# Performance work log

Measured on AMD Instinct MI355X. Metric: run time of the kernel, lower is better.

## Reference

```python
import jax, jax.numpy as jnp
import numpy as np

BINS = 256
MAXV = float(2 ** 14 - 1)
LAP_K = jnp.array([[0.0, 1.0, 0.0], [1.0, -4.0, 1.0], [0.0, 1.0, 0.0]], jnp.float32).reshape(1, 1, 3, 3)


def _soft_hist_entropy(flat):
    # flat: (B, N) in arbitrary range; per-image min-max normalize to [0,1]
    fmin = jnp.min(flat, axis=1, keepdims=True)
    fmax = jnp.max(flat, axis=1, keepdims=True)
    rng = fmax - fmin
    rng = jnp.where(rng == 0, jnp.ones_like(rng), rng)
    x = jnp.clip((flat - fmin) / rng, 0.0, 1.0)
    # Triangular soft-histogram weights clamp(1-|x-c_k|/bw, 0) are nonzero for at
    # most the 2 bins adjacent to x, so scatter-add instead of a (B,N,BINS) tensor.
    p = x * BINS - 0.5            # position in bin-center coordinates
    i0 = jnp.floor(p)
    w1 = p - i0                   # weight on bin i0+1
    w0 = 1.0 - w1                 # weight on bin i0
    i0i = i0.astype(jnp.int32)
    i1i = i0i + 1
    v0 = (i0i >= 0) & (i0i < BINS)
    v1 = (i1i >= 0) & (i1i < BINS)

    def hist_one(idx0, idx1, a0, a1, m0, m1):
        h = jnp.zeros((BINS,), flat.dtype)
        h = h.at[jnp.clip(idx0, 0, BINS - 1)].add(jnp.where(m0, a0, 0.0))
        h = h.at[jnp.clip(idx1, 0, BINS - 1)].add(jnp.where(m1, a1, 0.0))
        return h

    hist = jax.vmap(hist_one)(i0i, i1i, w0, w1, v0, v1)  # (B, BINS)
    hist = hist / (jnp.sum(hist, axis=1, keepdims=True) + 1e-10)
    ent = -jnp.sum(hist * jnp.log2(hist + 1e-10), axis=1)
    return ent / jnp.float32(np.log2(BINS))


def _extract_features(image):
    # normalize 14-bit input to [0,1] iff values exceed 1 (matches torch branch)
    image = jnp.where(jnp.max(image) > 1.0, image / MAXV, image)
    B = image.shape[0]
    flat = image.reshape(B, -1)
    variance = jnp.var(flat, axis=1, ddof=1)   # torch.var is unbiased
    mn = jnp.min(flat, axis=1)
    mx = jnp.max(flat, axis=1)
    ent = _soft_hist_entropy(flat)
    lap = jax.lax.conv_general_dilated(
        image, LAP_K, window_strides=(1, 1), padding=[(1, 1), (1, 1)],
        dimension_numbers=('NCHW', 'OIHW', 'NCHW'))
    lap_var = jnp.var(lap.reshape(B, -1), axis=1, ddof=1)
    return jnp.stack([variance, mn, mx, ent, lap_var], axis=1)  # (B, 5)


def setup_inputs() -> dict:
    key = jax.random.key(0)
    ks = jax.random.split(key, 4)
    image = jax.random.uniform(ks[0], (16, 1, 1024, 1280), jnp.float32) * MAXV
    # Kaiming normal fan_in (relu): std = sqrt(2 / fan_in); biases zero
    W1 = jax.random.normal(ks[1], (64, 5), jnp.float32) * np.float32(np.sqrt(2.0 / 5))
    W2 = jax.random.normal(ks[2], (64, 64), jnp.float32) * np.float32(np.sqrt(2.0 / 64))
    W3 = jax.random.normal(ks[3], (3, 64), jnp.float32) * np.float32(np.sqrt(2.0 / 64))
    return {
        'image': image,
        'W1': W1, 'b1': jnp.zeros((64,), jnp.float32),
        'W2': W2, 'b2': jnp.zeros((64,), jnp.float32),
        'W3': W3, 'b3': jnp.zeros((3,), jnp.float32),
    }


def reference(image, W1, b1, W2, b2, W3, b3):
    feats = _extract_features(image)                       # (B, 5)
    h = jax.nn.relu(feats @ W1.T + b1)
    h = jax.nn.relu(h @ W2.T + b2)
    logits = h @ W3.T + b3                                  # (B, 3)
    probs = jax.nn.softmax(logits, axis=1)
    class_ids = jnp.argmax(probs, axis=1)
    return class_ids, probs, feats
```

## Files before the change

kernel.cpp:

```cpp
#include <hip/hip_runtime.h>
#include <cfloat>
#include <math.h>

#define IMG_B 16
#define IMG_H 1024
#define IMG_W 1280
#define NPIX (IMG_H * IMG_W)
#define BINS 256
#define ROWS_PER_BLOCK 16
#define BLOCKS_PER_IMG_P1 (IMG_H / ROWS_PER_BLOCK)
#define T1 (IMG_W / 4)
#define BPI2 64
#define FIXP 65536.0f

__device__ __forceinline__ unsigned encf(float f) {
    unsigned u = __float_as_uint(f);
    return (u >> 31) ? ~u : (u | 0x80000000u);
}
__device__ __forceinline__ float decf(unsigned u) {
    unsigned b = (u & 0x80000000u) ? (u & 0x7fffffffu) : ~u;
    return __uint_as_float(b);
}


__global__ __launch_bounds__(256) void k_init(unsigned* mm, unsigned long long* hist64) {
    int t = blockIdx.x * 256 + threadIdx.x;
    hist64[t] = 0ull;
    if (t < IMG_B) { mm[2 * t] = 0xFFFFFFFFu; mm[2 * t + 1] = 0u; }
}

__global__ __launch_bounds__(T1) void k_pass1(const float* __restrict__ img,
                                              double* __restrict__ partials,
                                              unsigned* __restrict__ mm) {
    int blk = blockIdx.x;
    int b   = blk >> 6;
    int r0  = (blk & 63) * ROWS_PER_BLOCK;
    const float* base = img + (size_t)b * NPIX;
    int c = threadIdx.x;

    float fmn = FLT_MAX, fmx = -FLT_MAX;
    double s = 0.0, s2 = 0.0, ls = 0.0, ls2 = 0.0;

    for (int i = 0; i < ROWS_PER_BLOCK; ++i) {
        int r = r0 + i;
        const float* rowf = base + (size_t)r * IMG_W;
        float4 m = ((const float4*)rowf)[c];
        float4 up = make_float4(0.f, 0.f, 0.f, 0.f);
        float4 dn = make_float4(0.f, 0.f, 0.f, 0.f);
        if (r > 0)          up = ((const float4*)(rowf - IMG_W))[c];
        if (r < IMG_H - 1)  dn = ((const float4*)(rowf + IMG_W))[c];
        float lft = (c > 0)      ? rowf[4 * c - 1] : 0.f;
        float rgt = (c < T1 - 1) ? rowf[4 * c + 4] : 0.f;

        fmn = fminf(fmn, fminf(fminf(m.x, m.y), fminf(m.z, m.w)));
        fmx = fmaxf(fmx, fmaxf(fmaxf(m.x, m.y), fmaxf(m.z, m.w)));
        s  += (double)m.x + (double)m.y + (double)m.z + (double)m.w;
        s2 += (double)m.x * m.x + (double)m.y * m.y + (double)m.z * m.z + (double)m.w * m.w;

        float l0 = up.x + dn.x + lft + m.y - 4.f * m.x;
        float l1 = up.y + dn.y + m.x + m.z - 4.f * m.y;
        float l2 = up.z + dn.z + m.y + m.w - 4.f * m.z;
        float l3 = up.w + dn.w + m.z + rgt - 4.f * m.w;
        ls  += (double)l0 + (double)l1 + (double)l2 + (double)l3;
        ls2 += (double)l0 * l0 + (double)l1 * l1 + (double)l2 * l2 + (double)l3 * l3;
    }

    for (int o = 32; o; o >>= 1) {
        s   += __shfl_down(s,   (unsigned)o, 64);
        s2  += __shfl_down(s2,  (unsigned)o, 64);
        ls  += __shfl_down(ls,  (unsigned)o, 64);
        ls2 += __shfl_down(ls2, (unsigned)o, 64);
        fmn = fminf(fmn, __shfl_down(fmn, (unsigned)o, 64));
        fmx = fmaxf(fmx, __shfl_down(fmx, (unsigned)o, 64));
    }
    __shared__ double rd[4][5];
    __shared__ float  rf[2][5];
    int lane = threadIdx.x & 63, wv = threadIdx.x >> 6;
    if (lane == 0) {
        rd[0][wv] = s; rd[1][wv] = s2; rd[2][wv] = ls; rd[3][wv] = ls2;
        rf[0][wv] = fmn; rf[1][wv] = fmx;
    }
    __syncthreads();
    if (threadIdx.x == 0) {
        double S = 0, S2 = 0, LS = 0, LS2 = 0;
        float mn = FLT_MAX, mx = -FLT_MAX;
        for (int i = 0; i < 5; ++i) {
            S += rd[0][i]; S2 += rd[1][i]; LS += rd[2][i]; LS2 += rd[3][i];
            mn = fminf(mn, rf[0][i]); mx = fmaxf(mx, rf[1][i]);
        }
        double* p = partials + (size_t)blk * 4;
        p[0] = S; p[1] = S2; p[2] = LS; p[3] = LS2;
        atomicMin(&mm[b * 2 + 0], encf(mn));
        atomicMax(&mm[b * 2 + 1], encf(mx));
    }
}

__global__ __launch_bounds__(256) void k_pass2(const float* __restrict__ img,
                                               const unsigned* __restrict__ mm,
                                               unsigned long long* __restrict__ hist64) {
    __shared__ unsigned lh[BINS];
    int b     = blockIdx.x / BPI2;
    int blkin = blockIdx.x % BPI2;
    lh[threadIdx.x] = 0u;
    __syncthreads();

    float fmn = decf(mm[b * 2 + 0]);
    float fmx = decf(mm[b * 2 + 1]);
    float rng = fmx - fmn;
    if (rng == 0.f) rng = 1.f;
    float inv = 1.f / rng;

    const float4* p = (const float4*)(img + (size_t)b * NPIX);
    int nf4 = NPIX / 4;
    for (int i = blkin * 256 + threadIdx.x; i < nf4; i += BPI2 * 256) {
        float4 v = p[i];
        #pragma unroll
        for (int j = 0; j < 4; ++j) {
            float vv = (j == 0) ? v.x : (j == 1) ? v.y : (j == 2) ? v.z : v.w;
            float x  = fminf(fmaxf((vv - fmn) * inv, 0.f), 1.f);
            float pp = x * 256.f - 0.5f;
            float fi = floorf(pp);
            int   i0 = (int)fi;
            float w1 = pp - fi;
            unsigned w1q = (unsigned)(w1 * FIXP + 0.5f);
            unsigned w0q = 65536u - w1q;
            if (i0 >= 0)       atomicAdd(&lh[i0], w0q);
            if (i0 < BINS - 1) atomicAdd(&lh[i0 + 1], w1q);
        }
    }
    __syncthreads();
    unsigned hv = lh[threadIdx.x];
    if (hv != 0u)
        atomicAdd(&hist64[b * BINS + threadIdx.x], (unsigned long long)hv);
}

__global__ __launch_bounds__(256) void k_pass3(const unsigned long long* __restrict__ hist64,
                                               const double* __restrict__ partials,
                                               const unsigned* __restrict__ mm,
                                               float* __restrict__ featsw,
                                               float* __restrict__ out) {
    int b = blockIdx.x, t = threadIdx.x;
    double h = (double)hist64[b * BINS + t] * (1.0 / 65536.0);

    __shared__ double red[4];
    __shared__ float red2[4];
    __shared__ double mom[4];
    double tot = h;
    for (int o = 32; o; o >>= 1) tot += __shfl_down(tot, (unsigned)o, 64);
    if ((t & 63) == 0) red[t >> 6] = tot;

    if (t < 64) {
        const double* p = partials + ((size_t)b * 64 + t) * 4;
        double q0 = p[0], q1 = p[1], q2 = p[2], q3 = p[3];
        for (int o = 32; o; o >>= 1) {
            q0 += __shfl_down(q0, (unsigned)o, 64);
            q1 += __shfl_down(q1, (unsigned)o, 64);
            q2 += __shfl_down(q2, (unsigned)o, 64);
            q3 += __shfl_down(q3, (unsigned)o, 64);
        }
        if (t == 0) { mom[0] = q0; mom[1] = q1; mom[2] = q2; mom[3] = q3; }
    }
    __syncthreads();
    double tot_all = red[0] + red[1] + red[2] + red[3];

    float hn = (float)(h / (tot_all + 1e-10));
    float ce = hn * log2f(hn + 1e-10f);
    for (int o = 32; o; o >>= 1) ce += __shfl_down(ce, (unsigned)o, 64);
    if ((t & 63) == 0) red2[t >> 6] = ce;
    __syncthreads();

    if (t == 0) {
        float ent = -(red2[0] + red2[1] + red2[2] + red2[3]) / 8.f;
        float gmax = -FLT_MAX;
        for (int i = 0; i < IMG_B; ++i) gmax = fmaxf(gmax, decf(mm[i * 2 + 1]));
        float sc = (gmax > 1.f) ? (1.f / 16383.f) : 1.f;
        double N = (double)NPIX;
        double S = mom[0], S2 = mom[1], LS = mom[2], LS2 = mom[3];
        double sc2 = (double)sc * (double)sc;
        float var  = (float)((S2  - S  * S  / N) / (N - 1.0) * sc2);
        float lvar = (float)((LS2 - LS * LS / N) / (N - 1.0) * sc2);
        float mn = decf(mm[b * 2 + 0]) * sc;
        float mx = decf(mm[b * 2 + 1]) * sc;
        float* fo = out + 16 + 48 + b * 5;
        fo[0] = var; fo[1] = mn; fo[2] = mx; fo[3] = ent; fo[4] = lvar;
        float* fw = featsw + b * 5;
        fw[0] = var; fw[1] = mn; fw[2] = mx; fw[3] = ent; fw[4] = lvar;
    }
}

__global__ __launch_bounds__(64) void k_pass4(const float* __restrict__ feats,
                                              const float* __restrict__ W1, const float* __restrict__ b1,
                                              const float* __restrict__ W2, const float* __restrict__ b2,
                                              const float* __restrict__ W3, const float* __restrict__ b3,
                                              float* __restrict__ out) {
    int t = threadIdx.x;
    int b = blockIdx.x;
    __shared__ float f[5], h1[64], h2[64], lg[3];
    if (t < 5) f[t] = feats[b * 5 + t];
    __syncthreads();
    float a = b1[t];
    #pragma unroll
    for (int k = 0; k < 5; ++k) a += W1[t * 5 + k] * f[k];
    h1[t] = fmaxf(a, 0.f);
    __syncthreads();
    float a2 = b2[t];
    #pragma unroll
    for (int k = 0; k < 64; ++k) a2 += W2[t * 64 + k] * h1[k];
    h2[t] = fmaxf(a2, 0.f);
    __syncthreads();
    if (t < 3) {
        float a3 = b3[t];
        #pragma unroll
        for (int k = 0; k < 64; ++k) a3 += W3[t * 64 + k] * h2[k];
        lg[t] = a3;
    }
    __syncthreads();
    if (t == 0) {
        float m = fmaxf(lg[0], fmaxf(lg[1], lg[2]));
        float e0 = expf(lg[0] - m), e1 = expf(lg[1] - m), e2 = expf(lg[2] - m);
        float inv = 1.f / (e0 + e1 + e2);
        float p0 = e0 * inv, p1 = e1 * inv, p2 = e2 * inv;
        out[16 + b * 3 + 0] = p0;
        out[16 + b * 3 + 1] = p1;
        out[16 + b * 3 + 2] = p2;
        int cid = 0; float bm = p0;
        if (p1 > bm) { bm = p1; cid = 1; }
        if (p2 > bm) { bm = p2; cid = 2; }
        out[b] = (float)cid;
    }
}

extern "C" void kernel_launch(void* const* d_in, const int* in_sizes, int n_in,
                              void* d_out, int out_size, void* d_ws, size_t ws_size,
                              hipStream_t stream) {
    const float* img = (const float*)d_in[0];
    const float* W1  = (const float*)d_in[1];
    const float* b1  = (const float*)d_in[2];
    const float* W2  = (const float*)d_in[3];
    const float* b2  = (const float*)d_in[4];
    const float* W3  = (const float*)d_in[5];
    const float* b3  = (const float*)d_in[6];
    float* out = (float*)d_out;

    char* ws = (char*)d_ws;
    double*             partials = (double*)ws;
    unsigned*           mm       = (unsigned*)(ws + 32768);
    unsigned long long* hist64   = (unsigned long long*)(ws + 32896);
    float*              featsw   = (float*)(ws + 65664);

    k_init <<<16, 256, 0, stream>>>(mm, hist64);
    k_pass1<<<IMG_B * BLOCKS_PER_IMG_P1, T1, 0, stream>>>(img, partials, mm);
    k_pass2<<<IMG_B * BPI2, 256, 0, stream>>>(img, mm, hist64);
    k_pass3<<<IMG_B, 256, 0, stream>>>(hist64, partials, mm, featsw, out);
    k_pass4<<<IMG_B, 64, 0, stream>>>(featsw, W1, b1, W2, b2, W3, b3, out);
}
```

Baseline: 175.1 us.

## Fuse all passes into one cooperative kernel with grid syncs

Replaces the five-kernel chain with a single cooperative kernel of 1024 blocks that uses grid.sync between the moments/min-max stage, the histogram stage and the per-image finalize plus MLP head. Per-block partial histograms and min/max are written to workspace and reduced by the finalize blocks, which removes the global 64-bit atomics and the init kernel. The moment pass now accumulates in float per thread with register rows and wave shuffles for the left/right neighbours instead of double accumulation. This trades launch overhead and atomics for grid-wide barriers, reduced-precision partial sums, and a dependence on the cooperative launch succeeding; the old path remains as a fallback.

```diff
diff --git a/kernel.cpp b/kernel.cpp
--- a/kernel.cpp
+++ b/kernel.cpp
@@ -1,16 +1,17 @@
 #include <hip/hip_runtime.h>
+#include <hip/hip_cooperative_groups.h>
 #include <cfloat>
 #include <math.h>
+
+namespace cg = cooperative_groups;
 
 #define IMG_B 16
 #define IMG_H 1024
 #define IMG_W 1280
 #define NPIX (IMG_H * IMG_W)
 #define BINS 256
-#define ROWS_PER_BLOCK 16
-#define BLOCKS_PER_IMG_P1 (IMG_H / ROWS_PER_BLOCK)
-#define T1 (IMG_W / 4)
-#define BPI2 64
+#define NBLK 1024
+#define NTHR 256
 #define FIXP 65536.0f
 
 __device__ __forceinline__ unsigned encf(float f) {
@@ -22,6 +23,258 @@
     return __uint_as_float(b);
 }
 
+
+__global__ __launch_bounds__(NTHR, 4) void k_fused(
+    const float* __restrict__ img,
+    const float* __restrict__ W1, const float* __restrict__ b1,
+    const float* __restrict__ W2, const float* __restrict__ b2,
+    const float* __restrict__ W3, const float* __restrict__ b3,
+    float* __restrict__ out,
+    double* __restrict__ mom, uint2* __restrict__ mmp,
+    unsigned* __restrict__ bhist)
+{
+    cg::grid_group grid = cg::this_grid();
+    const int blk  = blockIdx.x;
+    const int tid  = threadIdx.x;
+    const int b    = blk >> 6;
+    const int sl   = blk & 63;
+    const int lane = tid & 63;
+    const int wv   = tid >> 6;
+
+    __shared__ float    swred[6][4];
+    __shared__ unsigned lh[BINS];
+    __shared__ float    sh_mm[2];
+    __shared__ double   dred[4];
+    __shared__ float    fred[4];
+    __shared__ double   smom[4];
+    __shared__ unsigned smm2[2];
+    __shared__ unsigned sgm[4];
+    __shared__ float    f5[5], h1[64], h2[64], lg[3];
+
+    const float* base = img + (size_t)b * NPIX;
+
+    {
+        float fs = 0.f, fs2 = 0.f, fls = 0.f, fls2 = 0.f;
+        float fmn = FLT_MAX, fmx = -FLT_MAX;
+
+        const int r0 = sl * 16 + wv * 4;
+        const float4* rp = (const float4*)(base + (size_t)r0 * IMG_W);
+        float4 up[5], m[5], dn[5];
+        #pragma unroll
+        for (int k = 0; k < 5; ++k) {
+            int c = k * 64 + lane;
+            up[k] = (r0 > 0) ? rp[c - 320] : make_float4(0.f, 0.f, 0.f, 0.f);
+            m[k]  = rp[c];
+        }
+        #pragma unroll
+        for (int i = 0; i < 4; ++i) {
+            int r = r0 + i;
+            const float4* nr = (const float4*)(base + (size_t)(r + 1) * IMG_W);
+            #pragma unroll
+            for (int k = 0; k < 5; ++k)
+                dn[k] = (r < IMG_H - 1) ? nr[k * 64 + lane]
+                                        : make_float4(0.f, 0.f, 0.f, 0.f);
+            #pragma unroll
+            for (int k = 0; k < 5; ++k) {
+                float4 mm = m[k], u = up[k], d = dn[k];
+                float lin  = __shfl_up(mm.w, 1u, 64);
+                float lwr  = m[k ? k - 1 : 0].w;
+                lwr = __shfl(lwr, 63, 64);
+                float lft  = (lane == 0) ? ((k > 0) ? lwr : 0.f) : lin;
+                float rin  = __shfl_down(mm.x, 1u, 64);
+                float rwr  = m[k < 4 ? k + 1 : 4].x;
+                rwr = __shfl(rwr, 0, 64);
+                float rgt  = (lane == 63) ? ((k < 4) ? rwr : 0.f) : rin;
+
+                float l0 = u.x + d.x + lft  + mm.y - 4.f * mm.x;
+                float l1 = u.y + d.y + mm.x + mm.z - 4.f * mm.y;
+                float l2 = u.z + d.z + mm.y + mm.w - 4.f * mm.z;
+                float l3 = u.w + d.w + mm.z + rgt  - 4.f * mm.w;
+
+                fs   += (mm.x + mm.y) + (mm.z + mm.w);
+                fs2  += mm.x * mm.x + mm.y * mm.y + mm.z * mm.z + mm.w * mm.w;
+                fls  += (l0 + l1) + (l2 + l3);
+                fls2 += l0 * l0 + l1 * l1 + l2 * l2 + l3 * l3;
+                fmn = fminf(fmn, fminf(fminf(mm.x, mm.y), fminf(mm.z, mm.w)));
+                fmx = fmaxf(fmx, fmaxf(fmaxf(mm.x, mm.y), fmaxf(mm.z, mm.w)));
+            }
+            #pragma unroll
+            for (int k = 0; k < 5; ++k) { up[k] = m[k]; m[k] = dn[k]; }
+        }
+
+        for (int o = 32; o; o >>= 1) {
+            fs   += __shfl_down(fs,   (unsigned)o, 64);
+            fs2  += __shfl_down(fs2,  (unsigned)o, 64);
+            fls  += __shfl_down(fls,  (unsigned)o, 64);
+            fls2 += __shfl_down(fls2, (unsigned)o, 64);
+            fmn = fminf(fmn, __shfl_down(fmn, (unsigned)o, 64));
+            fmx = fmaxf(fmx, __shfl_down(fmx, (unsigned)o, 64));
+        }
+        if (lane == 0) {
+            swred[0][wv] = fs;  swred[1][wv] = fs2;
+            swred[2][wv] = fls; swred[3][wv] = fls2;
+            swred[4][wv] = fmn; swred[5][wv] = fmx;
+        }
+        __syncthreads();
+        if (tid == 0) {
+            double S = 0, S2 = 0, LS = 0, LS2 = 0;
+            float mn = FLT_MAX, mx = -FLT_MAX;
+            for (int i = 0; i < 4; ++i) {
+                S  += (double)swred[0][i]; S2  += (double)swred[1][i];
+                LS += (double)swred[2][i]; LS2 += (double)swred[3][i];
+                mn = fminf(mn, swred[4][i]); mx = fmaxf(mx, swred[5][i]);
+            }
+            mom[blk * 4 + 0] = S;  mom[blk * 4 + 1] = S2;
+            mom[blk * 4 + 2] = LS; mom[blk * 4 + 3] = LS2;
+            mmp[blk] = make_uint2(encf(mn), encf(mx));
+        }
+    }
+    __threadfence();
+    grid.sync();
+
+    {
+        if (tid < 64) {
+            uint2 e = mmp[b * 64 + tid];
+            unsigned emn = e.x, emx = e.y;
+            for (int o = 32; o; o >>= 1) {
+                emn = min(emn, (unsigned)__shfl_down(emn, (unsigned)o, 64));
+                emx = max(emx, (unsigned)__shfl_down(emx, (unsigned)o, 64));
+            }
+            if (tid == 0) { sh_mm[0] = decf(emn); sh_mm[1] = decf(emx); }
+        }
+        lh[tid] = 0u;
+        __syncthreads();
+
+        float fmn = sh_mm[0], fmx = sh_mm[1];
+        float rng = fmx - fmn;
+        if (rng == 0.f) rng = 1.f;
+        float inv = 1.f / rng;
+
+        const float4* p = (const float4*)base + (size_t)sl * 5120;
+        #pragma unroll 4
+        for (int i = tid; i < 5120; i += NTHR) {
+            float4 v = p[i];
+            #pragma unroll
+            for (int j = 0; j < 4; ++j) {
+                float vv = (j == 0) ? v.x : (j == 1) ? v.y : (j == 2) ? v.z : v.w;
+                float x  = fminf(fmaxf((vv - fmn) * inv, 0.f), 1.f);
+                float pp = x * 256.f - 0.5f;
+                float fi = floorf(pp);
+                int   i0 = (int)fi;
+                float w1 = pp - fi;
+                unsigned w1q = (unsigned)(w1 * FIXP + 0.5f);
+                unsigned w0q = 65536u - w1q;
+                if (i0 >= 0)        atomicAdd(&lh[i0], w0q);
+                if (i0 < BINS - 1)  atomicAdd(&lh[i0 + 1], w1q);
+            }
+        }
+        __syncthreads();
+        bhist[blk * BINS + tid] = lh[tid];
+    }
+    __threadfence();
+    grid.sync();
+
+    if (blk >= IMG_B) return;
+    const int ib = blk;
+
+    double h = 0.0;
+    for (int s = 0; s < 64; ++s)
+        h += (double)bhist[(ib * 64 + s) * BINS + tid];
+
+    double tot = h;
+    for (int o = 32; o; o >>= 1) tot += __shfl_down(tot, (unsigned)o, 64);
+    if (lane == 0) dred[wv] = tot;
+    __syncthreads();
+    tot = dred[0] + dred[1] + dred[2] + dred[3];
+
+    double hv = h * (1.0 / 65536.0);
+    double tv = tot * (1.0 / 65536.0);
+    float hn = (float)(hv / (tv + 1e-10));
+    float ce = hn * log2f(hn + 1e-10f);
+    for (int o = 32; o; o >>= 1) ce += __shfl_down(ce, (unsigned)o, 64);
+    if (lane == 0) fred[wv] = ce;
+
+    if (tid < 64) {
+        double q0 = mom[(ib * 64 + tid) * 4 + 0];
+        double q1 = mom[(ib * 64 + tid) * 4 + 1];
+        double q2 = mom[(ib * 64 + tid) * 4 + 2];
+        double q3 = mom[(ib * 64 + tid) * 4 + 3];
+        uint2 e = mmp[ib * 64 + tid];
+        unsigned emn = e.x, emx = e.y;
+        for (int o = 32; o; o >>= 1) {
+            q0 += __shfl_down(q0, (unsigned)o, 64);
+            q1 += __shfl_down(q1, (unsigned)o, 64);
+            q2 += __shfl_down(q2, (unsigned)o, 64);
+            q3 += __shfl_down(q3, (unsigned)o, 64);
+            emn = min(emn, (unsigned)__shfl_down(emn, (unsigned)o, 64));
+            emx = max(emx, (unsigned)__shfl_down(emx, (unsigned)o, 64));
+        }
+        if (tid == 0) {
+            smom[0] = q0; smom[1] = q1; smom[2] = q2; smom[3] = q3;
+            smm2[0] = emn; smm2[1] = emx;
+        }
+    }
+    {
+        unsigned g = max(max(mmp[tid].y, mmp[256 + tid].y),
+                         max(mmp[512 + tid].y, mmp[768 + tid].y));
+        for (int o = 32; o; o >>= 1)
+            g = max(g, (unsigned)__shfl_down(g, (unsigned)o, 64));
+        if (lane == 0) sgm[wv] = g;
+    }
+    __syncthreads();
+
+    if (tid == 0) {
+        float ent = -(fred[0] + fred[1] + fred[2] + fred[3]) / 8.f;
+        float gmax = decf(max(max(sgm[0], sgm[1]), max(sgm[2], sgm[3])));
+        float sc = (gmax > 1.f) ? (1.f / 16383.f) : 1.f;
+        double N = (double)NPIX;
+        double S = smom[0], S2 = smom[1], LS = smom[2], LS2 = smom[3];
+        double sc2 = (double)sc * (double)sc;
+        float var  = (float)((S2  - S  * S  / N) / (N - 1.0) * sc2);
+        float lvar = (float)((LS2 - LS * LS / N) / (N - 1.0) * sc2);
+        float mn = decf(smm2[0]) * sc;
+        float mx = decf(smm2[1]) * sc;
+        float* fo = out + 64 + ib * 5;
+        fo[0] = var; fo[1] = mn; fo[2] = mx; fo[3] = ent; fo[4] = lvar;
+        f5[0] = var; f5[1] = mn; f5[2] = mx; f5[3] = ent; f5[4] = lvar;
+    }
+    __syncthreads();
+
+    if (tid < 64) {
+        float a = b1[tid];
+        #pragma unroll
+        for (int k = 0; k < 5; ++k) a += W1[tid * 5 + k] * f5[k];
+        h1[tid] = fmaxf(a, 0.f);
+    }
+    __syncthreads();
+    if (tid < 64) {
+        float a2 = b2[tid];
+        #pragma unroll
+        for (int k = 0; k < 64; ++k) a2 += W2[tid * 64 + k] * h1[k];
+        h2[tid] = fmaxf(a2, 0.f);
+    }
+    __syncthreads();
+    if (tid < 3) {
+        float a3 = b3[tid];
+        #pragma unroll
+        for (int k = 0; k < 64; ++k) a3 += W3[tid * 64 + k] * h2[k];
+        lg[tid] = a3;
+    }
+    __syncthreads();
+    if (tid == 0) {
+        float m = fmaxf(lg[0], fmaxf(lg[1], lg[2]));
+        float e0 = expf(lg[0] - m), e1 = expf(lg[1] - m), e2 = expf(lg[2] - m);
+        float inv = 1.f / (e0 + e1 + e2);
+        float p0 = e0 * inv, p1 = e1 * inv, p2 = e2 * inv;
+        out[16 + ib * 3 + 0] = p0;
+        out[16 + ib * 3 + 1] = p1;
+        out[16 + ib * 3 + 2] = p2;
+        int cid = 0; float bm = p0;
+        if (p1 > bm) { bm = p1; cid = 1; }
+        if (p2 > bm) { bm = p2; cid = 2; }
+        out[ib] = (float)cid;
+    }
+}
 
 __global__ __launch_bounds__(256) void k_init(unsigned* mm, unsigned long long* hist64) {
     int t = blockIdx.x * 256 + threadIdx.x;
@@ -29,19 +282,19 @@
     if (t < IMG_B) { mm[2 * t] = 0xFFFFFFFFu; mm[2 * t + 1] = 0u; }
 }
 
-__global__ __launch_bounds__(T1) void k_pass1(const float* __restrict__ img,
-                                              double* __restrict__ partials,
-                                              unsigned* __restrict__ mm) {
+__global__ __launch_bounds__(320) void k_pass1(const float* __restrict__ img,
+                                               double* __restrict__ partials,
+                                               unsigned* __restrict__ mm) {
     int blk = blockIdx.x;
     int b   = blk >> 6;
-    int r0  = (blk & 63) * ROWS_PER_BLOCK;
+    int r0  = (blk & 63) * 16;
     const float* base = img + (size_t)b * NPIX;
     int c = threadIdx.x;
 
     float fmn = FLT_MAX, fmx = -FLT_MAX;
     double s = 0.0, s2 = 0.0, ls = 0.0, ls2 = 0.0;
 
-    for (int i = 0; i < ROWS_PER_BLOCK; ++i) {
+    for (int i = 0; i < 16; ++i) {
         int r = r0 + i;
         const float* rowf = base + (size_t)r * IMG_W;
         float4 m = ((const float4*)rowf)[c];
@@ -49,8 +302,8 @@
         float4 dn = make_float4(0.f, 0.f, 0.f, 0.f);
         if (r > 0)          up = ((const float4*)(rowf - IMG_W))[c];
         if (r < IMG_H - 1)  dn = ((const float4*)(rowf + IMG_W))[c];
-        float lft = (c > 0)      ? rowf[4 * c - 1] : 0.f;
-        float rgt = (c < T1 - 1) ? rowf[4 * c + 4] : 0.f;
+        float lft = (c > 0)   ? rowf[4 * c - 1] : 0.f;
+        float rgt = (c < 319) ? rowf[4 * c + 4] : 0.f;
 
         fmn = fminf(fmn, fminf(fminf(m.x, m.y), fminf(m.z, m.w)));
         fmx = fmaxf(fmx, fmaxf(fmaxf(m.x, m.y), fmaxf(m.z, m.w)));
@@ -64,7 +317,6 @@
         ls  += (double)l0 + (double)l1 + (double)l2 + (double)l3;
         ls2 += (double)l0 * l0 + (double)l1 * l1 + (double)l2 * l2 + (double)l3 * l3;
     }
-
     for (int o = 32; o; o >>= 1) {
         s   += __shfl_down(s,   (unsigned)o, 64);
         s2  += __shfl_down(s2,  (unsigned)o, 64);
@@ -99,20 +351,17 @@
                                                const unsigned* __restrict__ mm,
                                                unsigned long long* __restrict__ hist64) {
     __shared__ unsigned lh[BINS];
-    int b     = blockIdx.x / BPI2;
-    int blkin = blockIdx.x % BPI2;
+    int b     = blockIdx.x / 64;
+    int blkin = blockIdx.x % 64;
     lh[threadIdx.x] = 0u;
     __syncthreads();
-
     float fmn = decf(mm[b * 2 + 0]);
     float fmx = decf(mm[b * 2 + 1]);
     float rng = fmx - fmn;
     if (rng == 0.f) rng = 1.f;
     float inv = 1.f / rng;
-
     const float4* p = (const float4*)(img + (size_t)b * NPIX);
-    int nf4 = NPIX / 4;
-    for (int i = blkin * 256 + threadIdx.x; i < nf4; i += BPI2 * 256) {
+    for (int i = blkin * 256 + threadIdx.x; i < NPIX / 4; i += 64 * 256) {
         float4 v = p[i];
         #pragma unroll
         for (int j = 0; j < 4; ++j) {
@@ -141,14 +390,12 @@
                                                float* __restrict__ out) {
     int b = blockIdx.x, t = threadIdx.x;
     double h = (double)hist64[b * BINS + t] * (1.0 / 65536.0);
-
     __shared__ double red[4];
     __shared__ float red2[4];
-    __shared__ double mom[4];
+    __shared__ double momx[4];
     double tot = h;
     for (int o = 32; o; o >>= 1) tot += __shfl_down(tot, (unsigned)o, 64);
     if ((t & 63) == 0) red[t >> 6] = tot;
-
     if (t < 64) {
         const double* p = partials + ((size_t)b * 64 + t) * 4;
         double q0 = p[0], q1 = p[1], q2 = p[2], q3 = p[3];
@@ -158,30 +405,28 @@
             q2 += __shfl_down(q2, (unsigned)o, 64);
             q3 += __shfl_down(q3, (unsigned)o, 64);
         }
-        if (t == 0) { mom[0] = q0; mom[1] = q1; mom[2] = q2; mom[3] = q3; }
+        if (t == 0) { momx[0] = q0; momx[1] = q1; momx[2] = q2; momx[3] = q3; }
     }
     __syncthreads();
     double tot_all = red[0] + red[1] + red[2] + red[3];
-
     float hn = (float)(h / (tot_all + 1e-10));
     float ce = hn * log2f(hn + 1e-10f);
     for (int o = 32; o; o >>= 1) ce += __shfl_down(ce, (unsigned)o, 64);
     if ((t & 63) == 0) red2[t >> 6] = ce;
     __syncthreads();
-
     if (t == 0) {
         float ent = -(red2[0] + red2[1] + red2[2] + red2[3]) / 8.f;
         float gmax = -FLT_MAX;
         for (int i = 0; i < IMG_B; ++i) gmax = fmaxf(gmax, decf(mm[i * 2 + 1]));
         float sc = (gmax > 1.f) ? (1.f / 16383.f) : 1.f;
         double N = (double)NPIX;
-        double S = mom[0], S2 = mom[1], LS = mom[2], LS2 = mom[3];
+        double S = momx[0], S2 = momx[1], LS = momx[2], LS2 = momx[3];
         double sc2 = (double)sc * (double)sc;
         float var  = (float)((S2  - S  * S  / N) / (N - 1.0) * sc2);
         float lvar = (float)((LS2 - LS * LS / N) / (N - 1.0) * sc2);
         float mn = decf(mm[b * 2 + 0]) * sc;
         float mx = decf(mm[b * 2 + 1]) * sc;
-        float* fo = out + 16 + 48 + b * 5;
+        float* fo = out + 64 + b * 5;
         fo[0] = var; fo[1] = mn; fo[2] = mx; fo[3] = ent; fo[4] = lvar;
         float* fw = featsw + b * 5;
         fw[0] = var; fw[1] = mn; fw[2] = mx; fw[3] = ent; fw[4] = lvar;
@@ -243,14 +488,25 @@
     float* out = (float*)d_out;
 
     char* ws = (char*)d_ws;
-    double*             partials = (double*)ws;
-    unsigned*           mm       = (unsigned*)(ws + 32768);
-    unsigned long long* hist64   = (unsigned long long*)(ws + 32896);
-    float*              featsw   = (float*)(ws + 65664);
-
-    k_init <<<16, 256, 0, stream>>>(mm, hist64);
-    k_pass1<<<IMG_B * BLOCKS_PER_IMG_P1, T1, 0, stream>>>(img, partials, mm);
-    k_pass2<<<IMG_B * BPI2, 256, 0, stream>>>(img, mm, hist64);
-    k_pass3<<<IMG_B, 256, 0, stream>>>(hist64, partials, mm, featsw, out);
-    k_pass4<<<IMG_B, 64, 0, stream>>>(featsw, W1, b1, W2, b2, W3, b3, out);
-}
+    double*   mom   = (double*)ws;
+    uint2*    mmp   = (uint2*)(ws + 32768);
+    unsigned* bhist = (unsigned*)(ws + 40960);
+
+    void* kargs[] = {(void*)&img, (void*)&W1, (void*)&b1, (void*)&W2, (void*)&b2,
+                     (void*)&W3, (void*)&b3, (void*)&out, (void*)&mom, (void*)&mmp,
+                     (void*)&bhist};
+    hipError_t err = hipLaunchCooperativeKernel((const void*)k_fused,
+                                                dim3(NBLK), dim3(NTHR),
+                                                kargs, 0, stream);
+    if (err != hipSuccess) {
+        double*             partials = (double*)ws;
+        unsigned*           mm       = (unsigned*)(ws + 32768);
+        unsigned long long* hist64   = (unsigned long long*)(ws + 32896);
+        float*              featsw   = (float*)(ws + 65664);
+        k_init <<<16, 256, 0, stream>>>(mm, hist64);
+        k_pass1<<<IMG_B * 64, 320, 0, stream>>>(img, partials, mm);
+        k_pass2<<<IMG_B * 64, 256, 0, stream>>>(img, mm, hist64);
+        k_pass3<<<IMG_B, 256, 0, stream>>>(hist64, partials, mm, featsw, out);
+        k_pass4<<<IMG_B, 64, 0, stream>>>(featsw, W1, b1, W2, b2, W3, b3, out);
+    }
+}
```

Measured after the change: 596.9 us. +241.0%, slower.

## Restructure pipeline into minmax, fused moments+histogram, and fused final kernel

Applied to the files above, without the earlier changes.

Splits the work into a light min/max pass and a main pass that computes moments, Laplacian moments and the soft histogram from one read of each pixel, removing the separate histogram pass over the image. Global atomics and the init kernel are replaced by per-block partial outputs that the final kernel reduces, and the feature and MLP kernels are merged into one. Moment accumulation moves from double to float per thread, which cuts double-precision cost but may lose accuracy. The image is still read twice in total, but the second read is shared between the statistics and histogram work.

```diff
diff --git a/kernel.cpp b/kernel.cpp
--- a/kernel.cpp
+++ b/kernel.cpp
@@ -7,10 +7,9 @@
 #define IMG_W 1280
 #define NPIX (IMG_H * IMG_W)
 #define BINS 256
-#define ROWS_PER_BLOCK 16
-#define BLOCKS_PER_IMG_P1 (IMG_H / ROWS_PER_BLOCK)
-#define T1 (IMG_W / 4)
-#define BPI2 64
+#define SLICES 64
+#define NBLK (IMG_B * SLICES)
+#define F4_PER_SLICE (16 * IMG_W / 4)
 #define FIXP 65536.0f
 
 __device__ __forceinline__ unsigned encf(float f) {
@@ -23,100 +22,98 @@
 }
 
 
-__global__ __launch_bounds__(256) void k_init(unsigned* mm, unsigned long long* hist64) {
-    int t = blockIdx.x * 256 + threadIdx.x;
-    hist64[t] = 0ull;
-    if (t < IMG_B) { mm[2 * t] = 0xFFFFFFFFu; mm[2 * t + 1] = 0u; }
-}
-
-__global__ __launch_bounds__(T1) void k_pass1(const float* __restrict__ img,
-                                              double* __restrict__ partials,
-                                              unsigned* __restrict__ mm) {
-    int blk = blockIdx.x;
-    int b   = blk >> 6;
-    int r0  = (blk & 63) * ROWS_PER_BLOCK;
+__global__ __launch_bounds__(256) void k_minmax(const float* __restrict__ img,
+                                                uint2* __restrict__ mmp) {
+    const int blk = blockIdx.x;
+    const int tid = threadIdx.x;
+    const float4* p = (const float4*)img + (size_t)blk * F4_PER_SLICE;
+
+    float fmn = FLT_MAX, fmx = -FLT_MAX;
+    #pragma unroll 4
+    for (int i = tid; i < F4_PER_SLICE; i += 256) {
+        float4 v = p[i];
+        fmn = fminf(fmn, fminf(fminf(v.x, v.y), fminf(v.z, v.w)));
+        fmx = fmaxf(fmx, fmaxf(fmaxf(v.x, v.y), fmaxf(v.z, v.w)));
+    }
+    for (int o = 32; o; o >>= 1) {
+        fmn = fminf(fmn, __shfl_down(fmn, (unsigned)o, 64));
+        fmx = fmaxf(fmx, __shfl_down(fmx, (unsigned)o, 64));
+    }
+    __shared__ float rmn[4], rmx[4];
+    int lane = tid & 63, wv = tid >> 6;
+    if (lane == 0) { rmn[wv] = fmn; rmx[wv] = fmx; }
+    __syncthreads();
+    if (tid == 0) {
+        float mn = fminf(fminf(rmn[0], rmn[1]), fminf(rmn[2], rmn[3]));
+        float mx = fmaxf(fmaxf(rmx[0], rmx[1]), fmaxf(rmx[2], rmx[3]));
+        mmp[blk] = make_uint2(encf(mn), encf(mx));
+    }
+}
+
+__global__ __launch_bounds__(256) void k_main(const float* __restrict__ img,
+                                              const uint2* __restrict__ mmp,
+                                              double* __restrict__ mom,
+                                              unsigned* __restrict__ bhist) {
+    const int blk = blockIdx.x;
+    const int tid = threadIdx.x;
+    const int b   = blk >> 6;
+    const int sl  = blk & 63;
+    const int lane = tid & 63, wv = tid >> 6;
+
+    __shared__ unsigned lh[BINS];
+    __shared__ float sh_mm[2];
+    __shared__ float swred[4][4];
+
+    if (tid < 64) {
+        uint2 e = mmp[b * 64 + tid];
+        unsigned emn = e.x, emx = e.y;
+        for (int o = 32; o; o >>= 1) {
+            emn = min(emn, (unsigned)__shfl_down(emn, (unsigned)o, 64));
+            emx = max(emx, (unsigned)__shfl_down(emx, (unsigned)o, 64));
+        }
+        if (tid == 0) { sh_mm[0] = decf(emn); sh_mm[1] = decf(emx); }
+    }
+    lh[tid] = 0u;
+    __syncthreads();
+
+    const float fmn = sh_mm[0], fmx = sh_mm[1];
+    float rng = fmx - fmn;
+    if (rng == 0.f) rng = 1.f;
+    const float inv = 1.f / rng;
+
     const float* base = img + (size_t)b * NPIX;
-    int c = threadIdx.x;
-
-    float fmn = FLT_MAX, fmx = -FLT_MAX;
-    double s = 0.0, s2 = 0.0, ls = 0.0, ls2 = 0.0;
-
-    for (int i = 0; i < ROWS_PER_BLOCK; ++i) {
-        int r = r0 + i;
+    const int r0 = sl * 16;
+
+    float fs = 0.f, fs2 = 0.f, fls = 0.f, fls2 = 0.f;
+
+    #pragma unroll 2
+    for (int k = 0; k < 20; ++k) {
+        int i   = tid + k * 256;
+        int ri  = i / 320;
+        int c   = i - ri * 320;
+        int r   = r0 + ri;
         const float* rowf = base + (size_t)r * IMG_W;
         float4 m = ((const float4*)rowf)[c];
         float4 up = make_float4(0.f, 0.f, 0.f, 0.f);
         float4 dn = make_float4(0.f, 0.f, 0.f, 0.f);
         if (r > 0)          up = ((const float4*)(rowf - IMG_W))[c];
         if (r < IMG_H - 1)  dn = ((const float4*)(rowf + IMG_W))[c];
-        float lft = (c > 0)      ? rowf[4 * c - 1] : 0.f;
-        float rgt = (c < T1 - 1) ? rowf[4 * c + 4] : 0.f;
-
-        fmn = fminf(fmn, fminf(fminf(m.x, m.y), fminf(m.z, m.w)));
-        fmx = fmaxf(fmx, fmaxf(fmaxf(m.x, m.y), fmaxf(m.z, m.w)));
-        s  += (double)m.x + (double)m.y + (double)m.z + (double)m.w;
-        s2 += (double)m.x * m.x + (double)m.y * m.y + (double)m.z * m.z + (double)m.w * m.w;
+        float lft = (c > 0)   ? rowf[4 * c - 1] : 0.f;
+        float rgt = (c < 319) ? rowf[4 * c + 4] : 0.f;
+
+        fs  += (m.x + m.y) + (m.z + m.w);
+        fs2 += (m.x * m.x + m.y * m.y) + (m.z * m.z + m.w * m.w);
 
         float l0 = up.x + dn.x + lft + m.y - 4.f * m.x;
         float l1 = up.y + dn.y + m.x + m.z - 4.f * m.y;
         float l2 = up.z + dn.z + m.y + m.w - 4.f * m.z;
         float l3 = up.w + dn.w + m.z + rgt - 4.f * m.w;
-        ls  += (double)l0 + (double)l1 + (double)l2 + (double)l3;
-        ls2 += (double)l0 * l0 + (double)l1 * l1 + (double)l2 * l2 + (double)l3 * l3;
-    }
-
-    for (int o = 32; o; o >>= 1) {
-        s   += __shfl_down(s,   (unsigned)o, 64);
-        s2  += __shfl_down(s2,  (unsigned)o, 64);
-        ls  += __shfl_down(ls,  (unsigned)o, 64);
-        ls2 += __shfl_down(ls2, (unsigned)o, 64);
-        fmn = fminf(fmn, __shfl_down(fmn, (unsigned)o, 64));
-        fmx = fmaxf(fmx, __shfl_down(fmx, (unsigned)o, 64));
-    }
-    __shared__ double rd[4][5];
-    __shared__ float  rf[2][5];
-    int lane = threadIdx.x & 63, wv = threadIdx.x >> 6;
-    if (lane == 0) {
-        rd[0][wv] = s; rd[1][wv] = s2; rd[2][wv] = ls; rd[3][wv] = ls2;
-        rf[0][wv] = fmn; rf[1][wv] = fmx;
-    }
-    __syncthreads();
-    if (threadIdx.x == 0) {
-        double S = 0, S2 = 0, LS = 0, LS2 = 0;
-        float mn = FLT_MAX, mx = -FLT_MAX;
-        for (int i = 0; i < 5; ++i) {
-            S += rd[0][i]; S2 += rd[1][i]; LS += rd[2][i]; LS2 += rd[3][i];
-            mn = fminf(mn, rf[0][i]); mx = fmaxf(mx, rf[1][i]);
-        }
-        double* p = partials + (size_t)blk * 4;
-        p[0] = S; p[1] = S2; p[2] = LS; p[3] = LS2;
-        atomicMin(&mm[b * 2 + 0], encf(mn));
-        atomicMax(&mm[b * 2 + 1], encf(mx));
-    }
-}
-
-__global__ __launch_bounds__(256) void k_pass2(const float* __restrict__ img,
-                                               const unsigned* __restrict__ mm,
-                                               unsigned long long* __restrict__ hist64) {
-    __shared__ unsigned lh[BINS];
-    int b     = blockIdx.x / BPI2;
-    int blkin = blockIdx.x % BPI2;
-    lh[threadIdx.x] = 0u;
-    __syncthreads();
-
-    float fmn = decf(mm[b * 2 + 0]);
-    float fmx = decf(mm[b * 2 + 1]);
-    float rng = fmx - fmn;
-    if (rng == 0.f) rng = 1.f;
-    float inv = 1.f / rng;
-
-    const float4* p = (const float4*)(img + (size_t)b * NPIX);
-    int nf4 = NPIX / 4;
-    for (int i = blkin * 256 + threadIdx.x; i < nf4; i += BPI2 * 256) {
-        float4 v = p[i];
+        fls  += (l0 + l1) + (l2 + l3);
+        fls2 += (l0 * l0 + l1 * l1) + (l2 * l2 + l3 * l3);
+
         #pragma unroll
         for (int j = 0; j < 4; ++j) {
-            float vv = (j == 0) ? v.x : (j == 1) ? v.y : (j == 2) ? v.z : v.w;
+            float vv = (j == 0) ? m.x : (j == 1) ? m.y : (j == 2) ? m.z : m.w;
             float x  = fminf(fmaxf((vv - fmn) * inv, 0.f), 1.f);
             float pp = x * 256.f - 0.5f;
             float fi = floorf(pp);
@@ -124,109 +121,148 @@
             float w1 = pp - fi;
             unsigned w1q = (unsigned)(w1 * FIXP + 0.5f);
             unsigned w0q = 65536u - w1q;
-            if (i0 >= 0)       atomicAdd(&lh[i0], w0q);
-            if (i0 < BINS - 1) atomicAdd(&lh[i0 + 1], w1q);
-        }
-    }
-    __syncthreads();
-    unsigned hv = lh[threadIdx.x];
-    if (hv != 0u)
-        atomicAdd(&hist64[b * BINS + threadIdx.x], (unsigned long long)hv);
-}
-
-__global__ __launch_bounds__(256) void k_pass3(const unsigned long long* __restrict__ hist64,
-                                               const double* __restrict__ partials,
-                                               const unsigned* __restrict__ mm,
-                                               float* __restrict__ featsw,
-                                               float* __restrict__ out) {
-    int b = blockIdx.x, t = threadIdx.x;
-    double h = (double)hist64[b * BINS + t] * (1.0 / 65536.0);
-
-    __shared__ double red[4];
-    __shared__ float red2[4];
-    __shared__ double mom[4];
+            if (i0 >= 0)        atomicAdd(&lh[i0], w0q);
+            if (i0 < BINS - 1)  atomicAdd(&lh[i0 + 1], w1q);
+        }
+    }
+
+    for (int o = 32; o; o >>= 1) {
+        fs   += __shfl_down(fs,   (unsigned)o, 64);
+        fs2  += __shfl_down(fs2,  (unsigned)o, 64);
+        fls  += __shfl_down(fls,  (unsigned)o, 64);
+        fls2 += __shfl_down(fls2, (unsigned)o, 64);
+    }
+    if (lane == 0) {
+        swred[0][wv] = fs;  swred[1][wv] = fs2;
+        swred[2][wv] = fls; swred[3][wv] = fls2;
+    }
+    __syncthreads();
+    if (tid == 0) {
+        double S  = (double)swred[0][0] + (double)swred[0][1] + (double)swred[0][2] + (double)swred[0][3];
+        double S2 = (double)swred[1][0] + (double)swred[1][1] + (double)swred[1][2] + (double)swred[1][3];
+        double LS  = (double)swred[2][0] + (double)swred[2][1] + (double)swred[2][2] + (double)swred[2][3];
+        double LS2 = (double)swred[3][0] + (double)swred[3][1] + (double)swred[3][2] + (double)swred[3][3];
+        mom[blk * 4 + 0] = S;  mom[blk * 4 + 1] = S2;
+        mom[blk * 4 + 2] = LS; mom[blk * 4 + 3] = LS2;
+    }
+    bhist[blk * BINS + tid] = lh[tid];
+}
+
+__global__ __launch_bounds__(256) void k_final(
+    const unsigned* __restrict__ bhist, const double* __restrict__ mom,
+    const uint2* __restrict__ mmp,
+    const float* __restrict__ W1, const float* __restrict__ b1,
+    const float* __restrict__ W2, const float* __restrict__ b2,
+    const float* __restrict__ W3, const float* __restrict__ b3,
+    float* __restrict__ out)
+{
+    const int ib = blockIdx.x;
+    const int tid = threadIdx.x;
+    const int lane = tid & 63, wv = tid >> 6;
+
+    __shared__ double dred[4];
+    __shared__ float  fred[4];
+    __shared__ double smom[4];
+    __shared__ unsigned smm2[2];
+    __shared__ unsigned sgm[4];
+    __shared__ float f5[5], h1[64], h2[64], lg[3];
+
+    double h = 0.0;
+    for (int s = 0; s < 64; ++s)
+        h += (double)bhist[(ib * 64 + s) * BINS + tid];
+
     double tot = h;
     for (int o = 32; o; o >>= 1) tot += __shfl_down(tot, (unsigned)o, 64);
-    if ((t & 63) == 0) red[t >> 6] = tot;
-
-    if (t < 64) {
-        const double* p = partials + ((size_t)b * 64 + t) * 4;
-        double q0 = p[0], q1 = p[1], q2 = p[2], q3 = p[3];
+    if (lane == 0) dred[wv] = tot;
+    __syncthreads();
+    tot = dred[0] + dred[1] + dred[2] + dred[3];
+
+    double hv = h * (1.0 / 65536.0);
+    double tv = tot * (1.0 / 65536.0);
+    float hn = (float)(hv / (tv + 1e-10));
+    float ce = hn * log2f(hn + 1e-10f);
+    for (int o = 32; o; o >>= 1) ce += __shfl_down(ce, (unsigned)o, 64);
+    if (lane == 0) fred[wv] = ce;
+
+    if (tid < 64) {
+        double q0 = mom[(ib * 64 + tid) * 4 + 0];
+        double q1 = mom[(ib * 64 + tid) * 4 + 1];
+        double q2 = mom[(ib * 64 + tid) * 4 + 2];
+        double q3 = mom[(ib * 64 + tid) * 4 + 3];
+        uint2 e = mmp[ib * 64 + tid];
+        unsigned emn = e.x, emx = e.y;
         for (int o = 32; o; o >>= 1) {
             q0 += __shfl_down(q0, (unsigned)o, 64);
             q1 += __shfl_down(q1, (unsigned)o, 64);
             q2 += __shfl_down(q2, (unsigned)o, 64);
             q3 += __shfl_down(q3, (unsigned)o, 64);
-        }
-        if (t == 0) { mom[0] = q0; mom[1] = q1; mom[2] = q2; mom[3] = q3; }
-    }
-    __syncthreads();
-    double tot_all = red[0] + red[1] + red[2] + red[3];
-
-    float hn = (float)(h / (tot_all + 1e-10));
-    float ce = hn * log2f(hn + 1e-10f);
-    for (int o = 32; o; o >>= 1) ce += __shfl_down(ce, (unsigned)o, 64);
-    if ((t & 63) == 0) red2[t >> 6] = ce;
-    __syncthreads();
-
-    if (t == 0) {
-        float ent = -(red2[0] + red2[1] + red2[2] + red2[3]) / 8.f;
-        float gmax = -FLT_MAX;
-        for (int i = 0; i < IMG_B; ++i) gmax = fmaxf(gmax, decf(mm[i * 2 + 1]));
+            emn = min(emn, (unsigned)__shfl_down(emn, (unsigned)o, 64));
+            emx = max(emx, (unsigned)__shfl_down(emx, (unsigned)o, 64));
+        }
+        if (tid == 0) {
+            smom[0] = q0; smom[1] = q1; smom[2] = q2; smom[3] = q3;
+            smm2[0] = emn; smm2[1] = emx;
+        }
+    }
+    {
+        unsigned g = max(max(mmp[tid].y, mmp[256 + tid].y),
+                         max(mmp[512 + tid].y, mmp[768 + tid].y));
+        for (int o = 32; o; o >>= 1)
+            g = max(g, (unsigned)__shfl_down(g, (unsigned)o, 64));
+        if (lane == 0) sgm[wv] = g;
+    }
+    __syncthreads();
+
+    if (tid == 0) {
+        float ent = -(fred[0] + fred[1] + fred[2] + fred[3]) / 8.f;
+        float gmax = decf(max(max(sgm[0], sgm[1]), max(sgm[2], sgm[3])));
         float sc = (gmax > 1.f) ? (1.f / 16383.f) : 1.f;
         double N = (double)NPIX;
-        double S = mom[0], S2 = mom[1], LS = mom[2], LS2 = mom[3];
+        double S = smom[0], S2 = smom[1], LS = smom[2], LS2 = smom[3];
         double sc2 = (double)sc * (double)sc;
         float var  = (float)((S2  - S  * S  / N) / (N - 1.0) * sc2);
         float lvar = (float)((LS2 - LS * LS / N) / (N - 1.0) * sc2);
-        float mn = decf(mm[b * 2 + 0]) * sc;
-        float mx = decf(mm[b * 2 + 1]) * sc;
-        float* fo = out + 16 + 48 + b * 5;
+        float mn = decf(smm2[0]) * sc;
+        float mx = decf(smm2[1]) * sc;
+        float* fo = out + 64 + ib * 5;
         fo[0] = var; fo[1] = mn; fo[2] = mx; fo[3] = ent; fo[4] = lvar;
-        float* fw = featsw + b * 5;
-        fw[0] = var; fw[1] = mn; fw[2] = mx; fw[3] = ent; fw[4] = lvar;
-    }
-}
-
-__global__ __launch_bounds__(64) void k_pass4(const float* __restrict__ feats,
-                                              const float* __restrict__ W1, const float* __restrict__ b1,
-                                              const float* __restrict__ W2, const float* __restrict__ b2,
-                                              const float* __restrict__ W3, const float* __restrict__ b3,
-                                              float* __restrict__ out) {
-    int t = threadIdx.x;
-    int b = blockIdx.x;
-    __shared__ float f[5], h1[64], h2[64], lg[3];
-    if (t < 5) f[t] = feats[b * 5 + t];
-    __syncthreads();
-    float a = b1[t];
-    #pragma unroll
-    for (int k = 0; k < 5; ++k) a += W1[t * 5 + k] * f[k];
-    h1[t] = fmaxf(a, 0.f);
-    __syncthreads();
-    float a2 = b2[t];
-    #pragma unroll
-    for (int k = 0; k < 64; ++k) a2 += W2[t * 64 + k] * h1[k];
-    h2[t] = fmaxf(a2, 0.f);
-    __syncthreads();
-    if (t < 3) {
-        float a3 = b3[t];
-        #pragma unroll
-        for (int k = 0; k < 64; ++k) a3 += W3[t * 64 + k] * h2[k];
-        lg[t] = a3;
-    }
-    __syncthreads();
-    if (t == 0) {
+        f5[0] = var; f5[1] = mn; f5[2] = mx; f5[3] = ent; f5[4] = lvar;
+    }
+    __syncthreads();
+
+    if (tid < 64) {
+        float a = b1[tid];
+        #pragma unroll
+        for (int k = 0; k < 5; ++k) a += W1[tid * 5 + k] * f5[k];
+        h1[tid] = fmaxf(a, 0.f);
+    }
+    __syncthreads();
+    if (tid < 64) {
+        float a2 = b2[tid];
+        #pragma unroll
+        for (int k = 0; k < 64; ++k) a2 += W2[tid * 64 + k] * h1[k];
+        h2[tid] = fmaxf(a2, 0.f);
+    }
+    __syncthreads();
+    if (tid < 3) {
+        float a3 = b3[tid];
+        #pragma unroll
+        for (int k = 0; k < 64; ++k) a3 += W3[tid * 64 + k] * h2[k];
+        lg[tid] = a3;
+    }
+    __syncthreads();
+    if (tid == 0) {
         float m = fmaxf(lg[0], fmaxf(lg[1], lg[2]));
         float e0 = expf(lg[0] - m), e1 = expf(lg[1] - m), e2 = expf(lg[2] - m);
         float inv = 1.f / (e0 + e1 + e2);
         float p0 = e0 * inv, p1 = e1 * inv, p2 = e2 * inv;
-        out[16 + b * 3 + 0] = p0;
-        out[16 + b * 3 + 1] = p1;
-        out[16 + b * 3 + 2] = p2;
+        out[16 + ib * 3 + 0] = p0;
+        out[16 + ib * 3 + 1] = p1;
+        out[16 + ib * 3 + 2] = p2;
         int cid = 0; float bm = p0;
         if (p1 > bm) { bm = p1; cid = 1; }
         if (p2 > bm) { bm = p2; cid = 2; }
-        out[b] = (float)cid;
+        out[ib] = (float)cid;
     }
 }
 
@@ -243,14 +279,12 @@
     float* out = (float*)d_out;
 
     char* ws = (char*)d_ws;
-    double*             partials = (double*)ws;
-    unsigned*           mm       = (unsigned*)(ws + 32768);
-    unsigned long long* hist64   = (unsigned long long*)(ws + 32896);
-    float*              featsw   = (float*)(ws + 65664);
-
-    k_init <<<16, 256, 0, stream>>>(mm, hist64);
-    k_pass1<<<IMG_B * BLOCKS_PER_IMG_P1, T1, 0, stream>>>(img, partials, mm);
-    k_pass2<<<IMG_B * BPI2, 256, 0, stream>>>(img, mm, hist64);
-    k_pass3<<<IMG_B, 256, 0, stream>>>(hist64, partials, mm, featsw, out);
-    k_pass4<<<IMG_B, 64, 0, stream>>>(featsw, W1, b1, W2, b2, W3, b3, out);
-}
+    uint2*    mmp   = (uint2*)ws;
+    double*   mom   = (double*)(ws + 8192);
+    unsigned* bhist = (unsigned*)(ws + 40960);
+
+    k_minmax<<<NBLK, 256, 0, stream>>>(img, mmp);
+    k_main  <<<NBLK, 256, 0, stream>>>(img, mmp, mom, bhist);
+    k_final <<<IMG_B, 256, 0, stream>>>(bhist, mom, mmp,
+                                        W1, b1, W2, b2, W3, b3, out);
+}
```

New measurement: 159.5 us. 8.9% less time.
